# Kernel optimization log

Measured on AMD Instinct MI355X. Metric: run time of the kernel, lower is better.

The kernel has to match this reference:

```python
import jax, jax.numpy as jnp
import numpy as np

N, E = 4096, 131072
D_IN, D_H, H, D_HEAD, D_OUT, L = 768, 256, 4, 64, 128, 2


def setup_inputs() -> dict:
    key = jax.random.key(0)
    ks = jax.random.split(key, 8)
    x = jax.random.normal(ks[0], (N, D_IN), dtype=jnp.float32)
    edge_index = jax.random.randint(ks[1], (2, E), 0, N, dtype=jnp.int64)
    Win = jax.random.normal(ks[2], (D_IN, D_H), dtype=jnp.float32) * 0.02
    bin_ = jnp.zeros((D_H,), dtype=jnp.float32)
    # per-layer, per-head projection weights [L, H, D_H, D_HEAD]
    Wg = jax.random.normal(ks[3], (L, H, D_H, D_HEAD), dtype=jnp.float32) * 0.05
    # per-layer, per-head attention vectors a: [L, H, 2*D_HEAD]
    a = jax.random.normal(ks[4], (L, H, 2 * D_HEAD), dtype=jnp.float32) * 0.05
    Wout = jax.random.normal(ks[5], (D_H, D_OUT), dtype=jnp.float32) * 0.05
    bout = jnp.zeros((D_OUT,), dtype=jnp.float32)
    return {"x": x, "edge_index": edge_index, "Win": Win, "bin_": bin_,
            "Wg": Wg, "a": a, "Wout": Wout, "bout": bout}


def _gat_layer(h, Wl, al, row, col):
    # h: [N, D_H], Wl: [H, D_H, D_HEAD], al: [H, 2*D_HEAD]
    hh = jnp.einsum('ni,hio->hno', h, Wl)          # [H, N, D_HEAD]
    a_src, a_dst = al[:, :D_HEAD], al[:, D_HEAD:]
    s_src = jnp.einsum('hno,ho->hn', hh, a_src)    # [H, N]
    s_dst = jnp.einsum('hno,ho->hn', hh, a_dst)    # [H, N]
    e = jax.nn.leaky_relu(s_src[:, row] + s_dst[:, col], negative_slope=0.2)  # [H, E]
    # dense scatter exactly as the torch module: zeros then assign at (row, col)
    att = jnp.zeros((H, N, N), dtype=h.dtype).at[:, row, col].set(e)
    att = jax.nn.softmax(att, axis=-1)             # dense row softmax (zeros included)
    hp = jnp.einsum('hnm,hmo->hno', att, hh)       # [H, N, D_HEAD]
    return jnp.transpose(hp, (1, 0, 2)).reshape(N, H * D_HEAD)


def reference(x, edge_index, Win, bin_, Wg, a, Wout, bout):
    row, col = edge_index[0], edge_index[1]
    h = jax.nn.relu(x @ Win + bin_)                # input_proj + relu (dropout = eval identity)
    for l in range(L):
        h = jax.nn.relu(_gat_layer(h, Wg[l], a[l], row, col))
    node_embeddings = h @ Wout + bout              # [N, D_OUT]
    return node_embeddings
```

## Files before the change

kernel.cpp:

```cpp
#include <hip/hip_runtime.h>
#include <hip/hip_bf16.h>

#define NNODES 4096
#define NEDGES 131072
#define D_IN   768
#define D_H    256
#define NHEAD  4
#define D_HEAD 64
#define D_OUT  128
#define DEGCAP 192
#define S_SCALE 1048576.0f

typedef __attribute__((ext_vector_type(4))) float f32x4;
typedef __attribute__((ext_vector_type(8))) short bf16x8;
typedef __attribute__((ext_vector_type(8))) unsigned short u16x8;

static __device__ __forceinline__ unsigned short f2bf(float f) {
    __hip_bfloat16 h = __float2bfloat16(f);
    return *reinterpret_cast<unsigned short*>(&h);
}
static __device__ __forceinline__ float bf2f(unsigned short u) {
    return __uint_as_float((unsigned)u << 16);
}

#define OFF_XB     (0u)
#define OFF_H0     (6u<<20)
#define OFF_H1     (8u<<20)
#define OFF_HH     (10u<<20)
#define OFF_SINT   (12u<<20)
#define OFF_SSRC   (OFF_SINT + 4096u)
#define OFF_SDST   (OFF_SSRC + 65536u)
#define OFF_WINT   (OFF_SDST + 65536u)
#define OFF_WGT    (OFF_WINT + 393216u)
#define OFF_WOUTT  (OFF_WGT + 262144u)
#define OFF_BM     (OFF_WOUTT + 65536u)

__global__ __launch_bounds__(256) void k_init(
    const float* __restrict__ Win, const float* __restrict__ Wg,
    const float* __restrict__ Wout, const float* __restrict__ x,
    unsigned short* __restrict__ WinT, unsigned short* __restrict__ WgT,
    unsigned short* __restrict__ WoutT, unsigned short* __restrict__ xb,
    uint4* __restrict__ bm4, unsigned long long* __restrict__ Sint)
{
    __shared__ float tile[32][33];
    const int tid = threadIdx.x, bid = blockIdx.x;
    bm4[bid*256 + tid] = make_uint4(0u,0u,0u,0u);
    if (bid == 0) { Sint[tid] = 0ull; Sint[256 + tid] = 0ull; }

    {
        const float4* x4 = (const float4*)x;
        ushort4* xb4 = (ushort4*)xb;
        for (int i = bid*256 + tid; i < (NNODES*D_IN)/4; i += 512*256) {
            float4 v = x4[i];
            ushort4 o;
            o.x = f2bf(v.x); o.y = f2bf(v.y); o.z = f2bf(v.z); o.w = f2bf(v.w);
            xb4[i] = o;
        }
    }

    if (bid < 352) {
        const float* src; unsigned short* dst; int R, Cc, tr, tc;
        if (bid < 192)      { src = Win;  dst = WinT;  R = 768; Cc = 256; tr = bid >> 3; tc = bid & 7; }
        else if (bid < 320) { int t = bid - 192; int m = t >> 4, s = t & 15;
                              src = Wg + (size_t)m*16384; dst = WgT + (size_t)m*16384;
                              R = 256; Cc = 64; tr = s >> 1; tc = s & 1; }
        else                { int t = bid - 320; src = Wout; dst = WoutT;
                              R = 256; Cc = 128; tr = t >> 2; tc = t & 3; }
        int ci = tid & 31, rq = tid >> 5;
        #pragma unroll
        for (int rr = rq; rr < 32; rr += 8)
            tile[rr][ci] = src[(size_t)(tr*32+rr)*Cc + tc*32 + ci];
        __syncthreads();
        int ri = tid & 31, cq = tid >> 5;
        #pragma unroll
        for (int cc = cq; cc < 32; cc += 8)
            dst[(size_t)(tc*32+cc)*R + tr*32 + ri] = f2bf(tile[ri][cc]);
    }
}

__global__ __launch_bounds__(256) void gemm_mfma(
    const unsigned short* __restrict__ A, const unsigned short* __restrict__ BT,
    const float* __restrict__ bias, float* __restrict__ Cf,
    unsigned short* __restrict__ Cb,
    int N, int K, int relu,
    const float* __restrict__ a_l, float* __restrict__ ssrc,
    float* __restrict__ sdst, unsigned long long* __restrict__ Sint,
    const int* __restrict__ ei, unsigned* __restrict__ bm)
{
    __shared__ unsigned short As[32][72];
    __shared__ unsigned short Bs[64][72];
    __shared__ float sredS[4][32], sredD[4][32];
    const int tid = threadIdx.x;
    int bx, by;
    if (ei) {
        int bid = blockIdx.x;
        int xcd = bid & 7, q = bid >> 3;
        bx = q & 3;
        by = (q >> 2)*8 + xcd;
    } else {
        bx = blockIdx.x; by = blockIdx.y;
    }
    const int wc = tid >> 6;
    const int lane = tid & 63;
    const int g = lane >> 4, c = lane & 15;
    const int ar = tid >> 3, ak = (tid & 7) * 8;
    const int bc = tid >> 2, bk = (tid & 3) * 16;
    f32x4 acc0 = {0.f,0.f,0.f,0.f}, acc1 = {0.f,0.f,0.f,0.f};
    const unsigned short* Arow = A + (size_t)(by*32 + ar)*K;
    const unsigned short* Brow = BT + (size_t)(bx*64 + bc)*K;

    for (int k0 = 0; k0 < K; k0 += 64) {
        u16x8 avv = *(const u16x8*)&Arow[k0 + ak];
        u16x8 bv0 = *(const u16x8*)&Brow[k0 + bk];
        u16x8 bv1 = *(const u16x8*)&Brow[k0 + bk + 8];
        *(u16x8*)&As[ar][ak]     = avv;
        *(u16x8*)&Bs[bc][bk]     = bv0;
        *(u16x8*)&Bs[bc][bk + 8] = bv1;
        __syncthreads();
        bf16x8 b0  = *(bf16x8*)&Bs[wc*16 + c][g*8];
        bf16x8 b1  = *(bf16x8*)&Bs[wc*16 + c][32 + g*8];
        bf16x8 a00 = *(bf16x8*)&As[c][g*8];
        bf16x8 a01 = *(bf16x8*)&As[c][32 + g*8];
        bf16x8 a10 = *(bf16x8*)&As[16 + c][g*8];
        bf16x8 a11 = *(bf16x8*)&As[16 + c][32 + g*8];
        acc0 = __builtin_amdgcn_mfma_f32_16x16x32_bf16(a00, b0, acc0, 0, 0, 0);
        acc0 = __builtin_amdgcn_mfma_f32_16x16x32_bf16(a01, b1, acc0, 0, 0, 0);
        acc1 = __builtin_amdgcn_mfma_f32_16x16x32_bf16(a10, b0, acc1, 0, 0, 0);
        acc1 = __builtin_amdgcn_mfma_f32_16x16x32_bf16(a11, b1, acc1, 0, 0, 0);
        __syncthreads();
    }

    const int col = bx*64 + wc*16 + c;
    float bb = bias ? bias[col] : 0.f;
    #pragma unroll
    for (int t = 0; t < 2; ++t) {
        f32x4 av = t ? acc1 : acc0;
        #pragma unroll
        for (int i = 0; i < 4; ++i) {
            int r = by*32 + t*16 + g*4 + i;
            float v = av[i] + bb;
            if (relu) v = fmaxf(v, 0.f);
            if (Cb) Cb[(size_t)r*N + col] = f2bf(v);
            else    Cf[(size_t)r*N + col] = v;
        }
    }

    if (a_l) {
        int h = bx;
        float as = a_l[h*128 + wc*16 + c];
        float ad = a_l[h*128 + 64 + wc*16 + c];
        float ps[8], pd[8], cs = 0.f;
        #pragma unroll
        for (int t = 0; t < 2; ++t) {
            f32x4 av = t ? acc1 : acc0;
            #pragma unroll
            for (int i = 0; i < 4; ++i) {
                ps[t*4+i] = av[i] * as;
                pd[t*4+i] = av[i] * ad;
                cs += av[i];
            }
        }
        #pragma unroll
        for (int off = 1; off < 16; off <<= 1) {
            #pragma unroll
            for (int j = 0; j < 8; ++j) {
                ps[j] += __shfl_xor(ps[j], off);
                pd[j] += __shfl_xor(pd[j], off);
            }
        }
        if (c == 0) {
            #pragma unroll
            for (int t = 0; t < 2; ++t)
                #pragma unroll
                for (int i = 0; i < 4; ++i) {
                    sredS[wc][t*16 + g*4 + i] = ps[t*4+i];
                    sredD[wc][t*16 + g*4 + i] = pd[t*4+i];
                }
        }
        cs += __shfl_xor(cs, 16);
        cs += __shfl_xor(cs, 32);
        if (g == 0) {
            long long q = (long long)llrintf(cs * S_SCALE);
            atomicAdd(&Sint[col], (unsigned long long)q);
        }
        __syncthreads();
        if (tid < 32) {
            float s1 = sredS[0][tid] + sredS[1][tid] + sredS[2][tid] + sredS[3][tid];
            float s2 = sredD[0][tid] + sredD[1][tid] + sredD[2][tid] + sredD[3][tid];
            int r = by*32 + tid;
            ssrc[r*4 + h] = s1;
            sdst[r*4 + h] = s2;
        }
    }

    if (ei) {
        __shared__ int flag;
        int bid = blockIdx.x;
        if (tid < 64) {
            int v = ei[2*tid + 1];
            unsigned long long ball = __ballot(v == 0);
            if (tid == 0) flag = (ball == ~0ull) ? 1 : 0;
        }
        __syncthreads();
        int is64 = flag;
        int k = bid*256 + tid;
        int r  = is64 ? ei[2*k]            : ei[k];
        int cc = is64 ? ei[2*NEDGES + 2*k] : ei[NEDGES + k];
        r &= (NNODES-1); cc &= (NNODES-1);
        atomicOr(&bm[(size_t)r*128 + (cc>>5)], 1u << (cc & 31));
    }
}

__global__ __launch_bounds__(256) void aggregate_kernel(
    const unsigned* __restrict__ bm,
    const float* __restrict__ ssrc, const float* __restrict__ sdst,
    const unsigned short* __restrict__ hh,
    const unsigned long long* __restrict__ Sint,
    unsigned short* __restrict__ hout)
{
    __shared__ int   csr_lds[DEGCAP];
    __shared__ float w_lds[4*DEGCAP];
    int n = blockIdx.x;
    int tid = threadIdx.x;
    int h = tid >> 6, o = tid & 63;
    const unsigned* brow = bm + (size_t)n*128;
    float Sv = (float)(long long)Sint[h*64 + o] * (1.0f / S_SCALE);

    unsigned wA = brow[2*o], wB = brow[2*o + 1];
    int cpc = __popc(wA) + __popc(wB);
    int pre = cpc;
    #pragma unroll
    for (int off = 1; off < 64; off <<= 1) {
        int v = __shfl_up(pre, off);
        if (o >= off) pre += v;
    }
    int excl = pre - cpc;
    int cnt = __shfl(pre, 63);
    if (cnt <= DEGCAP) {
        int pos = excl, base = o*64;
        unsigned w = wA;
        while (w) { int b = __builtin_ctz(w); csr_lds[pos++] = base + b; w &= w-1; }
        w = wB; base += 32;
        while (w) { int b = __builtin_ctz(w); csr_lds[pos++] = base + b; w &= w-1; }
    }
    float ss = ssrc[n*4 + h];

    if (cnt <= DEGCAP) {
        float mx = 0.f;
        for (int i = o; i < cnt; i += 64) {
            int m = csr_lds[i];
            float e = ss + sdst[m*4 + h];
            e = (e >= 0.f) ? e : 0.2f*e;
            w_lds[h*DEGCAP + i] = e;
            mx = fmaxf(mx, e);
        }
        #pragma unroll
        for (int off = 32; off; off >>= 1) mx = fmaxf(mx, __shfl_xor(mx, off));
        float M = mx;
        float base = expf(-M);

        float zp = 0.f;
        for (int i = o; i < cnt; i += 64) {
            float w = expf(w_lds[h*DEGCAP + i] - M) - base;
            w_lds[h*DEGCAP + i] = w;
            zp += w;
        }
        #pragma unroll
        for (int off = 32; off; off >>= 1) zp += __shfl_xor(zp, off);

        float acc = 0.f;
        int i = 0;
        for (; i + 8 <= cnt; i += 8) {
            int   mm[8]; float wq[8]; float vq[8];
            #pragma unroll
            for (int j = 0; j < 8; ++j) {
                mm[j] = csr_lds[i+j];
                wq[j] = w_lds[h*DEGCAP + i + j];
            }
            #pragma unroll
            for (int j = 0; j < 8; ++j)
                vq[j] = bf2f(hh[(size_t)mm[j]*256 + h*64 + o]);
            #pragma unroll
            for (int j = 0; j < 8; ++j)
                acc += wq[j] * vq[j];
        }
        for (; i < cnt; ++i)
            acc += w_lds[h*DEGCAP+i] * bf2f(hh[(size_t)csr_lds[i]*256 + h*64 + o]);

        float Z  = zp + (float)NNODES * base;
        float hp = (acc + base * Sv) / Z;
        hout[(size_t)n*256 + h*64 + o] = f2bf(fmaxf(hp, 0.f));
    } else {
        float mx = 0.f;
        for (int m = o; m < NNODES; m += 64) {
            if ((brow[m>>5] >> (m & 31)) & 1u) {
                float e = ss + sdst[m*4 + h];
                e = (e >= 0.f) ? e : 0.2f*e;
                mx = fmaxf(mx, e);
            }
        }
        #pragma unroll
        for (int off = 32; off; off >>= 1) mx = fmaxf(mx, __shfl_xor(mx, off));
        float M = mx;
        float base = expf(-M);
        float zp = 0.f, acc = 0.f;
        for (int m = 0; m < NNODES; ++m) {
            if ((brow[m>>5] >> (m & 31)) & 1u) {
                float e = ss + sdst[m*4 + h];
                e = (e >= 0.f) ? e : 0.2f*e;
                float w = expf(e - M) - base;
                zp += w;
                acc += w * bf2f(hh[(size_t)m*256 + h*64 + o]);
            }
        }
        float Z  = zp + (float)NNODES * base;
        float hp = (acc + base * Sv) / Z;
        hout[(size_t)n*256 + h*64 + o] = f2bf(fmaxf(hp, 0.f));
    }
}

static int find_size(const int* sz, int n, int want, int fallback)
{
    for (int i = 0; i < n; ++i) if (sz[i] == want) return i;
    return fallback;
}

extern "C" void kernel_launch(void* const* d_in, const int* in_sizes, int n_in,
                              void* d_out, int out_size, void* d_ws, size_t ws_size,
                              hipStream_t stream)
{
    int ix   = find_size(in_sizes, n_in, NNODES*D_IN, 0);
    int ie   = find_size(in_sizes, n_in, 2*NEDGES, 1);
    int iwin = find_size(in_sizes, n_in, D_IN*D_H, 2);
    int ibin = find_size(in_sizes, n_in, D_H, 3);
    int iwg  = find_size(in_sizes, n_in, 2*NHEAD*D_H*D_HEAD, 4);
    int ia   = find_size(in_sizes, n_in, 2*NHEAD*2*D_HEAD, 5);
    int iwo  = find_size(in_sizes, n_in, D_H*D_OUT, 6);
    int ibo  = find_size(in_sizes, n_in, D_OUT, 7);

    const float* x    = (const float*)d_in[ix];
    const int*   ei   = (const int*)d_in[ie];
    const float* Win  = (const float*)d_in[iwin];
    const float* bin_ = (const float*)d_in[ibin];
    const float* Wg   = (const float*)d_in[iwg];
    const float* a    = (const float*)d_in[ia];
    const float* Wout = (const float*)d_in[iwo];
    const float* bout = (const float*)d_in[ibo];
    float* out = (float*)d_out;

    char* ws = (char*)d_ws;
    unsigned short*     xb    = (unsigned short*)(ws + OFF_XB);
    unsigned short*     h0    = (unsigned short*)(ws + OFF_H0);
    unsigned short*     h1    = (unsigned short*)(ws + OFF_H1);
    unsigned short*     hh    = (unsigned short*)(ws + OFF_HH);
    unsigned long long* Sint  = (unsigned long long*)(ws + OFF_SINT);
    float*              ssrc  = (float*)(ws + OFF_SSRC);
    float*              sdst  = (float*)(ws + OFF_SDST);
    unsigned short*     WinT  = (unsigned short*)(ws + OFF_WINT);
    unsigned short*     WgT   = (unsigned short*)(ws + OFF_WGT);
    unsigned short*     WoutT = (unsigned short*)(ws + OFF_WOUTT);
    unsigned*           bm    = (unsigned*)(ws + OFF_BM);

    k_init<<<512, 256, 0, stream>>>(Win, Wg, Wout, x, WinT, WgT, WoutT, xb,
                                    (uint4*)bm, Sint);

    gemm_mfma<<<512, 256, 0, stream>>>(xb, WinT, bin_, nullptr, h0,
                                       D_H, D_IN, 1,
                                       nullptr, nullptr, nullptr, nullptr,
                                       ei, bm);

    unsigned short* hin = h0;
    unsigned short* hcur = h1;
    for (int l = 0; l < 2; ++l) {
        dim3 g2(D_H/64, NNODES/32);
        gemm_mfma<<<g2, 256, 0, stream>>>(hin, WgT + (size_t)l*NHEAD*D_HEAD*D_H,
                                          nullptr, nullptr, hh,
                                          D_H, D_H, 0,
                                          a + (size_t)l*NHEAD*128, ssrc, sdst,
                                          Sint + (size_t)l*256,
                                          nullptr, nullptr);
        aggregate_kernel<<<NNODES, 256, 0, stream>>>(bm, ssrc, sdst, hh,
                                                     Sint + (size_t)l*256, hcur);
        unsigned short* t = hin; hin = hcur; hcur = t;
    }

    {
        dim3 g(D_OUT/64, NNODES/32);
        gemm_mfma<<<g, 256, 0, stream>>>(hin, WoutT, bout, out, nullptr,
                                         D_OUT, D_H, 0,
                                         nullptr, nullptr, nullptr, nullptr,
                                         nullptr, nullptr);
    }
}
```

Baseline: 79.72 us.

## Drop softmax max pass and gather full 8-byte rows split across waves

```diff
diff --git a/kernel.cpp b/kernel.cpp
--- a/kernel.cpp
+++ b/kernel.cpp
@@ -220,11 +220,13 @@
 {
     __shared__ int   csr_lds[DEGCAP];
     __shared__ float w_lds[4*DEGCAP];
-    int n = blockIdx.x;
-    int tid = threadIdx.x;
-    int h = tid >> 6, o = tid & 63;
+    __shared__ float accs[4][256];
+    __shared__ float zp_sh[4];
+    const int n = blockIdx.x;
+    const int tid = threadIdx.x;
+    const int wv = tid >> 6, o = tid & 63;
     const unsigned* brow = bm + (size_t)n*128;
-    float Sv = (float)(long long)Sint[h*64 + o] * (1.0f / S_SCALE);
+    const float Sv = (float)(long long)Sint[tid] * (1.0f / S_SCALE);
 
     unsigned wA = brow[2*o], wB = brow[2*o + 1];
     int cpc = __popc(wA) + __popc(wB);
@@ -243,79 +245,76 @@
         w = wB; base += 32;
         while (w) { int b = __builtin_ctz(w); csr_lds[pos++] = base + b; w &= w-1; }
     }
-    float ss = ssrc[n*4 + h];
 
     if (cnt <= DEGCAP) {
-        float mx = 0.f;
+        float ss = ssrc[n*4 + wv];
+        float zp = 0.f;
         for (int i = o; i < cnt; i += 64) {
             int m = csr_lds[i];
-            float e = ss + sdst[m*4 + h];
+            float e = ss + sdst[m*4 + wv];
             e = (e >= 0.f) ? e : 0.2f*e;
-            w_lds[h*DEGCAP + i] = e;
-            mx = fmaxf(mx, e);
-        }
-        #pragma unroll
-        for (int off = 32; off; off >>= 1) mx = fmaxf(mx, __shfl_xor(mx, off));
-        float M = mx;
-        float base = expf(-M);
-
-        float zp = 0.f;
-        for (int i = o; i < cnt; i += 64) {
-            float w = expf(w_lds[h*DEGCAP + i] - M) - base;
-            w_lds[h*DEGCAP + i] = w;
+            float w = expf(e) - 1.0f;
+            w_lds[wv*DEGCAP + i] = w;
             zp += w;
         }
         #pragma unroll
         for (int off = 32; off; off >>= 1) zp += __shfl_xor(zp, off);
-
-        float acc = 0.f;
-        int i = 0;
-        for (; i + 8 <= cnt; i += 8) {
-            int   mm[8]; float wq[8]; float vq[8];
-            #pragma unroll
-            for (int j = 0; j < 8; ++j) {
-                mm[j] = csr_lds[i+j];
-                wq[j] = w_lds[h*DEGCAP + i + j];
-            }
-            #pragma unroll
-            for (int j = 0; j < 8; ++j)
-                vq[j] = bf2f(hh[(size_t)mm[j]*256 + h*64 + o]);
-            #pragma unroll
-            for (int j = 0; j < 8; ++j)
-                acc += wq[j] * vq[j];
-        }
-        for (; i < cnt; ++i)
-            acc += w_lds[h*DEGCAP+i] * bf2f(hh[(size_t)csr_lds[i]*256 + h*64 + o]);
-
-        float Z  = zp + (float)NNODES * base;
-        float hp = (acc + base * Sv) / Z;
-        hout[(size_t)n*256 + h*64 + o] = f2bf(fmaxf(hp, 0.f));
+        if (o == 0) zp_sh[wv] = zp;
+        __syncthreads();
+
+        const int h = o >> 4;
+        const int wbase = h*DEGCAP;
+        float a0 = 0.f, a1 = 0.f, a2 = 0.f, a3 = 0.f;
+        const unsigned short* hrow0 = hh + (size_t)o*4;
+        int i = wv;
+        for (; i + 12 < cnt; i += 16) {
+            int m0 = csr_lds[i],    m1 = csr_lds[i+4];
+            int m2 = csr_lds[i+8],  m3 = csr_lds[i+12];
+            float w0 = w_lds[wbase+i],   w1 = w_lds[wbase+i+4];
+            float w2 = w_lds[wbase+i+8], w3 = w_lds[wbase+i+12];
+            uint2 p0 = *(const uint2*)(hrow0 + (size_t)m0*256);
+            uint2 p1 = *(const uint2*)(hrow0 + (size_t)m1*256);
+            uint2 p2 = *(const uint2*)(hrow0 + (size_t)m2*256);
+            uint2 p3 = *(const uint2*)(hrow0 + (size_t)m3*256);
+            a0 += w0*bf2f((unsigned short)(p0.x&0xffffu)); a1 += w0*bf2f((unsigned short)(p0.x>>16));
+            a2 += w0*bf2f((unsigned short)(p0.y&0xffffu)); a3 += w0*bf2f((unsigned short)(p0.y>>16));
+            a0 += w1*bf2f((unsigned short)(p1.x&0xffffu)); a1 += w1*bf2f((unsigned short)(p1.x>>16));
+            a2 += w1*bf2f((unsigned short)(p1.y&0xffffu)); a3 += w1*bf2f((unsigned short)(p1.y>>16));
+            a0 += w2*bf2f((unsigned short)(p2.x&0xffffu)); a1 += w2*bf2f((unsigned short)(p2.x>>16));
+            a2 += w2*bf2f((unsigned short)(p2.y&0xffffu)); a3 += w2*bf2f((unsigned short)(p2.y>>16));
+            a0 += w3*bf2f((unsigned short)(p3.x&0xffffu)); a1 += w3*bf2f((unsigned short)(p3.x>>16));
+            a2 += w3*bf2f((unsigned short)(p3.y&0xffffu)); a3 += w3*bf2f((unsigned short)(p3.y>>16));
+        }
+        for (; i < cnt; i += 4) {
+            int m = csr_lds[i];
+            float w = w_lds[wbase+i];
+            uint2 p = *(const uint2*)(hrow0 + (size_t)m*256);
+            a0 += w*bf2f((unsigned short)(p.x&0xffffu)); a1 += w*bf2f((unsigned short)(p.x>>16));
+            a2 += w*bf2f((unsigned short)(p.y&0xffffu)); a3 += w*bf2f((unsigned short)(p.y>>16));
+        }
+        float4 av; av.x = a0; av.y = a1; av.z = a2; av.w = a3;
+        *(float4*)&accs[wv][o*4] = av;
+        __syncthreads();
+
+        float sum4 = accs[0][tid] + accs[1][tid] + accs[2][tid] + accs[3][tid];
+        float Z = zp_sh[tid >> 6] + (float)NNODES;
+        float hp = (sum4 + Sv) / Z;
+        hout[(size_t)n*256 + tid] = f2bf(fmaxf(hp, 0.f));
     } else {
-        float mx = 0.f;
-        for (int m = o; m < NNODES; m += 64) {
-            if ((brow[m>>5] >> (m & 31)) & 1u) {
-                float e = ss + sdst[m*4 + h];
-                e = (e >= 0.f) ? e : 0.2f*e;
-                mx = fmaxf(mx, e);
-            }
-        }
-        #pragma unroll
-        for (int off = 32; off; off >>= 1) mx = fmaxf(mx, __shfl_xor(mx, off));
-        float M = mx;
-        float base = expf(-M);
+        float ss = ssrc[n*4 + wv];
         float zp = 0.f, acc = 0.f;
         for (int m = 0; m < NNODES; ++m) {
             if ((brow[m>>5] >> (m & 31)) & 1u) {
-                float e = ss + sdst[m*4 + h];
+                float e = ss + sdst[m*4 + wv];
                 e = (e >= 0.f) ? e : 0.2f*e;
-                float w = expf(e - M) - base;
+                float w = expf(e) - 1.0f;
                 zp += w;
-                acc += w * bf2f(hh[(size_t)m*256 + h*64 + o]);
+                acc += w * bf2f(hh[(size_t)m*256 + wv*64 + o]);
             }
         }
-        float Z  = zp + (float)NNODES * base;
-        float hp = (acc + base * Sv) / Z;
-        hout[(size_t)n*256 + h*64 + o] = f2bf(fmaxf(hp, 0.f));
+        float Z  = zp + (float)NNODES;
+        float hp = (acc + Sv) / Z;
+        hout[(size_t)n*256 + wv*64 + o] = f2bf(fmaxf(hp, 0.f));
     }
 }
 
```

Result: faster. 72.09 us (-9.6%).
